# Optimization experiments

Measured on AMD Instinct MI355X. Metric: run time of the kernel, lower is better.

The kernel has to match this reference:

```python
import jax, jax.numpy as jnp
import numpy as np

N, G, E, F, H = 65536, 32768, 600000, 128, 128

def _mlp(x, w1, b1, w2, b2):
    # Linear -> SiLU -> Linear
    return jax.nn.silu(x @ w1 + b1) @ w2 + b2

def setup_inputs() -> dict:
    key = jax.random.key(0)
    ks = jax.random.split(key, 24)
    def lin(k, din, dout):
        kw, kb = jax.random.split(k)
        s = 1.0 / np.sqrt(din)
        return (jax.random.uniform(kw, (din, dout), jnp.float32, -s, s),
                jax.random.uniform(kb, (dout,), jnp.float32, -s, s))
    nm_w1, nm_b1 = lin(ks[0], F, H)
    nm_w2, nm_b2 = lin(ks[1], H, H)
    em_w1, em_b1 = lin(ks[2], 6, H)
    em_w2, em_b2 = lin(ks[3], H, H)
    mm_w1, mm_b1 = lin(ks[4], 2 * H, H)
    mm_w2, mm_b2 = lin(ks[5], H, H)
    um_w1, um_b1 = lin(ks[6], H, H)
    um_w2, um_b2 = lin(ks[7], H, H)
    return {
        "node_features": jax.random.normal(ks[8], (N, F), jnp.float32),
        "node_pos": jax.random.uniform(ks[9], (N, 3), jnp.float32),
        "grid_pos": jax.random.uniform(ks[10], (G, 3), jnp.float32),
        "edge_index": jax.random.randint(ks[11], (2, E), 0, G, jnp.int64),
        "nm_w1": nm_w1, "nm_b1": nm_b1, "nm_w2": nm_w2, "nm_b2": nm_b2,
        "em_w1": em_w1, "em_b1": em_b1, "em_w2": em_w2, "em_b2": em_b2,
        "mm_w1": mm_w1, "mm_b1": mm_b1, "mm_w2": mm_w2, "mm_b2": mm_b2,
        "um_w1": um_w1, "um_b1": um_b1, "um_w2": um_w2, "um_b2": um_b2,
    }

def reference(node_features, node_pos, grid_pos, edge_index,
              nm_w1, nm_b1, nm_w2, nm_b2,
              em_w1, em_b1, em_w2, em_b2,
              mm_w1, mm_b1, mm_w2, mm_b2,
              um_w1, um_b1, um_w2, um_b2):
    src, tgt = edge_index[0], edge_index[1]
    # node_model on all points [N,H]
    nf = _mlp(node_features, nm_w1, nm_b1, nm_w2, nm_b2)
    # edge features from gathered positions [E,6] -> [E,H]
    edge_attr = jnp.concatenate([node_pos[src], grid_pos[tgt]], axis=-1)
    ef = _mlp(edge_attr, em_w1, em_b1, em_w2, em_b2)
    # messages [E,2H] -> [E,H]
    msg = _mlp(jnp.concatenate([nf[src], ef], axis=-1), mm_w1, mm_b1, mm_w2, mm_b2)
    # scatter-add mean aggregation to grid [G,H]
    counts = jax.ops.segment_sum(jnp.ones((msg.shape[0],), msg.dtype), tgt, num_segments=G)
    counts = jnp.maximum(counts, 1.0)[:, None]
    agg = jax.ops.segment_sum(msg, tgt, num_segments=G) / counts
    # update_model [G,H]
    return _mlp(agg, um_w1, um_b1, um_w2, um_b2)
```

## Files before the change

kernel.cpp:

```cpp
#include <hip/hip_runtime.h>

#define N_NODES 65536
#define G_GRID  32768
#define E_EDGES 600000
#define HD      128

typedef __attribute__((ext_vector_type(8))) short bf8;
typedef __attribute__((ext_vector_type(4))) float f32x4;
typedef __attribute__((ext_vector_type(4))) unsigned u32x4;

__device__ __forceinline__ short f2bf(float f){
  union { float f; unsigned u; } v; v.f = f;
  unsigned r = v.u + 0x7FFFu + ((v.u >> 16) & 1u);
  return (short)(r >> 16);
}
__device__ __forceinline__ float bf2f(short s){
  union { unsigned u; float f; } v; v.u = ((unsigned)(unsigned short)s) << 16; return v.f;
}
__device__ __forceinline__ float fsilu(float v){
  return v * __builtin_amdgcn_rcpf(1.f + __expf(-v));
}
__device__ __forceinline__ unsigned cvt_pk_bf16(float lo, float hi){
  unsigned r;
  asm("v_cvt_pk_bf16_f32 %0, %1, %2" : "=v"(r) : "v"(lo), "v"(hi));
  return r;
}

__device__ __forceinline__ bf8 load_pack8(const float* p, float scale){
  float4 u0 = *(const float4*)p;
  float4 u1 = *(const float4*)(p + 4);
  u32x4 pk;
  pk[0] = cvt_pk_bf16(u0.x*scale, u0.y*scale);
  pk[1] = cvt_pk_bf16(u0.z*scale, u0.w*scale);
  pk[2] = cvt_pk_bf16(u1.x*scale, u1.y*scale);
  pk[3] = cvt_pk_bf16(u1.z*scale, u1.w*scale);
  return *(const bf8*)&pk;
}

__global__ void setup_k(const float* __restrict__ nmw1, const float* __restrict__ nmw2,
                        const float* __restrict__ mmw1, const float* __restrict__ mmw2,
                        const float* __restrict__ umw1, const float* __restrict__ umw2,
                        const float* __restrict__ emw1, const float* __restrict__ eb1,
                        const float* __restrict__ emw2, const float* __restrict__ eb2,
                        const float* __restrict__ mb1,
                        const int* __restrict__ eidx,
                        short* __restrict__ wts, short* __restrict__ wcombot,
                        float* __restrict__ bcombo, short* __restrict__ ew1x,
                        int* __restrict__ counts)
{
  const int b = blockIdx.x;
  if (b < 512){
    int i = b*256 + threadIdx.x;
    const float* src; int local; bool k256 = false;
    if      (i < 16384){ src = nmw1; local = i; }
    else if (i < 32768){ src = nmw2; local = i - 16384; }
    else if (i < 49152){ src = emw2; local = i - 32768; }
    else if (i < 81920){ src = mmw1; local = i - 49152; k256 = true; }
    else if (i < 98304){ src = mmw2; local = i - 81920; }
    else if (i < 114688){ src = umw1; local = i - 98304; }
    else               { src = umw2; local = i - 114688; }
    int n, k;
    if (k256){ n = local >> 8; k = local & 255; }
    else     { n = local >> 7; k = local & 127; }
    wts[i] = f2bf(src[k*HD + n]);
  } else if (b < 640){
    __shared__ float part[2][128];
    int k = b - 512;
    int t = threadIdx.x, n = t & 127, half = t >> 7;
    float acc = 0.f;
    const float* er = emw2 + k*HD + half*64;
    #pragma unroll 8
    for (int j=0;j<64;j++) acc += er[j] * mmw1[(HD + half*64 + j)*HD + n];
    part[half][n] = acc;
    __syncthreads();
    if (half == 0) wcombot[n*HD + k] = f2bf(part[0][n] + part[1][n]);
  } else if (b == 640){
    int t = threadIdx.x;
    if (t < 128){
      int n = t;
      float acc = mb1[n];
      for (int j=0;j<HD;j++) acc += eb2[j] * mmw1[(HD + j)*HD + n];
      bcombo[n] = acc;
      short v[32];
      #pragma unroll
      for (int i=0;i<32;i++) v[i] = 0;
      #pragma unroll
      for (int i=0;i<6;i++){
        float wv = emw1[i*HD + n];
        short wh = f2bf(wv);
        short wl = f2bf(wv - bf2f(wh));
        v[i] = wh; v[6+i] = wh; v[12+i] = wl;
      }
      float bv = eb1[n];
      short bh = f2bf(bv);
      v[18] = bh; v[19] = f2bf(bv - bf2f(bh));
      #pragma unroll
      for (int i=0;i<32;i++) ew1x[n*32 + i] = v[i];
    }
  } else {
    int e = (b - 641)*256 + threadIdx.x;
    if (e < E_EDGES) atomicAdd(&counts[eidx[E_EDGES + e]], 1);
  }
}

__global__ void node_mlp_k(const float* __restrict__ X,
                           const short* __restrict__ w1t, const float* __restrict__ b1,
                           const short* __restrict__ w2t, const float* __restrict__ b2,
                           short* __restrict__ nf)
{
  __shared__ short hid[64][136];
  const int t = threadIdx.x;
  const int wave = t >> 6, lane = t & 63, l15 = lane & 15, q = lane >> 4;
  const int rw = blockIdx.x*64 + wave*16;

  bf8 a[4];
  const float* xr = X + (size_t)(rw + l15)*HD;
  #pragma unroll
  for (int kt=0; kt<4; kt++) a[kt] = load_pack8(xr + kt*32 + q*8, 1.0f);

  #pragma unroll
  for (int ct=0; ct<8; ct++){
    f32x4 acc = {0.f,0.f,0.f,0.f};
    #pragma unroll
    for (int kt=0; kt<4; kt++){
      bf8 b = *(const bf8*)(w1t + (ct*16 + l15)*HD + kt*32 + q*8);
      acc = __builtin_amdgcn_mfma_f32_16x16x32_bf16(a[kt], b, acc, 0, 0, 0);
    }
    float bias = b1[ct*16 + l15];
    int col = ct*16 + l15;
    unsigned pa = cvt_pk_bf16(fsilu(acc[0]+bias), fsilu(acc[1]+bias));
    unsigned pb = cvt_pk_bf16(fsilu(acc[2]+bias), fsilu(acc[3]+bias));
    hid[wave*16 + q*4 + 0][col] = (short)(pa & 0xFFFFu);
    hid[wave*16 + q*4 + 1][col] = (short)(pa >> 16);
    hid[wave*16 + q*4 + 2][col] = (short)(pb & 0xFFFFu);
    hid[wave*16 + q*4 + 3][col] = (short)(pb >> 16);
  }
  bf8 a2[4];
  #pragma unroll
  for (int kt=0;kt<4;kt++) a2[kt] = *(const bf8*)&hid[wave*16 + l15][kt*32 + q*8];
  #pragma unroll
  for (int ct=0; ct<8; ct++){
    f32x4 acc = {0.f,0.f,0.f,0.f};
    #pragma unroll
    for (int kt=0;kt<4;kt++){
      bf8 b = *(const bf8*)(w2t + (ct*16 + l15)*HD + kt*32 + q*8);
      acc = __builtin_amdgcn_mfma_f32_16x16x32_bf16(a2[kt], b, acc, 0, 0, 0);
    }
    float bias = b2[ct*16 + l15];
    int col = ct*16 + l15;
    unsigned pa = cvt_pk_bf16(acc[0]+bias, acc[1]+bias);
    unsigned pb = cvt_pk_bf16(acc[2]+bias, acc[3]+bias);
    nf[(size_t)(rw + q*4 + 0)*HD + col] = (short)(pa & 0xFFFFu);
    nf[(size_t)(rw + q*4 + 1)*HD + col] = (short)(pa >> 16);
    nf[(size_t)(rw + q*4 + 2)*HD + col] = (short)(pb & 0xFFFFu);
    nf[(size_t)(rw + q*4 + 3)*HD + col] = (short)(pb >> 16);
  }
}

__global__ void scan_k(const int* __restrict__ counts, int* __restrict__ offs){
  __shared__ int part[1024];
  const int t = threadIdx.x;
  const int base = t*32;
  int loc[32];
  int s = 0;
  #pragma unroll
  for (int i=0;i<32;i++){ loc[i] = s; s += counts[base+i]; }
  part[t] = s;
  __syncthreads();
  for (int off=1; off<1024; off<<=1){
    int v = (t>=off) ? part[t-off] : 0;
    __syncthreads();
    part[t] += v;
    __syncthreads();
  }
  int pre = (t==0) ? 0 : part[t-1];
  #pragma unroll
  for (int i=0;i<32;i++) offs[base+i] = pre + loc[i];
  if (t==1023) offs[G_GRID] = pre + s;
}

__global__ void scatter_k(const int* __restrict__ eidx, const int* __restrict__ offs,
                          int* __restrict__ counts,
                          int* __restrict__ srcs_s, int* __restrict__ tgts_s,
                          const float* __restrict__ npos, const float* __restrict__ gpos,
                          float* __restrict__ pos6){
  int e = blockIdx.x*256 + threadIdx.x;
  if (e < E_EDGES){
    int s = eidx[e];
    int g = eidx[E_EDGES + e];
    int slot = offs[g] + atomicSub(&counts[g], 1) - 1;
    srcs_s[slot] = s;
    tgts_s[slot] = g;
    float* pd = pos6 + (size_t)slot*8;
    pd[0]=npos[s*3+0]; pd[1]=npos[s*3+1]; pd[2]=npos[s*3+2];
    pd[3]=gpos[g*3+0]; pd[4]=gpos[g*3+1]; pd[5]=gpos[g*3+2];
    pd[6]=0.f; pd[7]=0.f;
  }
}

__device__ __forceinline__ bf8 build_af(const float p[6], int q){
  short ph[6], pl[6];
  #pragma unroll
  for (int i=0;i<6;i++){
    ph[i] = f2bf(p[i]);
    pl[i] = f2bf(p[i] - bf2f(ph[i]));
  }
  bf8 af = {0,0,0,0,0,0,0,0};
  if (q == 0){
    af[0]=ph[0]; af[1]=ph[1]; af[2]=ph[2]; af[3]=ph[3];
    af[4]=ph[4]; af[5]=ph[5]; af[6]=pl[0]; af[7]=pl[1];
  } else if (q == 1){
    af[0]=pl[2]; af[1]=pl[3]; af[2]=pl[4]; af[3]=pl[5];
    af[4]=ph[0]; af[5]=ph[1]; af[6]=ph[2]; af[7]=ph[3];
  } else if (q == 2){
    af[0]=ph[4]; af[1]=ph[5]; af[2]=(short)0x3F80; af[3]=(short)0x3F80;
  }
  return af;
}

__device__ __forceinline__ void seg_flush32(const f32x4& a0, const f32x4& a1,
                                            unsigned m, int tr0, int tr1,
                                            int q, int col, bool owner,
                                            float* __restrict__ agg)
{
  if (m == 0u){
    float s = ((a0[0]+a0[1]) + (a0[2]+a0[3])) + ((a1[0]+a1[1]) + (a1[2]+a1[3]));
    s += __shfl_xor(s, 16);
    s += __shfl_xor(s, 32);
    int tg = __shfl(tr0, 0);
    if (owner) atomicAdd(&agg[(size_t)tg*HD + col], s);
  } else {
    unsigned mm = m;
    int lo = 0;
    while (true){
      int hi = mm ? (int)__builtin_ctz(mm) : 32;
      float s = 0.f;
      #pragma unroll
      for (int r=0;r<4;r++){
        int row0 = q*4 + r;
        int row1 = 16 + row0;
        s += (row0 >= lo && row0 < hi) ? a0[r] : 0.f;
        s += (row1 >= lo && row1 < hi) ? a1[r] : 0.f;
      }
      s += __shfl_xor(s, 16);
      s += __shfl_xor(s, 32);
      int tg = (lo < 16) ? __shfl(tr0, lo) : __shfl(tr1, lo - 16);
      if (owner) atomicAdd(&agg[(size_t)tg*HD + col], s);
      if (!mm) break;
      lo = hi; mm &= mm - 1;
    }
  }
}

__global__ void __launch_bounds__(256, 3)
edge_msg13_k(const int* __restrict__ srcs_s, const int* __restrict__ tgts_s,
             const float* __restrict__ pos6,
             const short* __restrict__ ew1x, const float* __restrict__ bcombo,
             const short* __restrict__ mw1t, const short* __restrict__ wcombot,
             const short* __restrict__ mw2t,
             const short* __restrict__ nf, float* __restrict__ agg)
{
  __shared__ int tgtl[128];
  __shared__ short hm[128][136];

  const int t = threadIdx.x;
  const int e0 = blockIdx.x*128;
  const int w = t >> 6, lane = t & 63, l15 = lane & 15, q = lane >> 4;
  const int base = e0 + w*32;
  if (base >= E_EDGES) return;

  const int i0 = base + l15;
  const int i1 = base + 16 + l15;
  const int s0 = srcs_s[i0], s1 = srcs_s[i1];

  bf8 an0[4], an1[4];
  {
    const short* n0p = nf + (size_t)s0*HD + q*8;
    const short* n1p = nf + (size_t)s1*HD + q*8;
    #pragma unroll
    for (int kt=0;kt<4;kt++){ an0[kt] = *(const bf8*)(n0p + kt*32); an1[kt] = *(const bf8*)(n1p + kt*32); }
  }
  float pA[6], pB[6];
  {
    const float* pp = pos6 + (size_t)i0*8;
    f32x4 u0 = *(const f32x4*)pp;
    f32x4 u1 = *(const f32x4*)(pp + 4);
    pA[0]=u0[0]; pA[1]=u0[1]; pA[2]=u0[2]; pA[3]=u0[3]; pA[4]=u1[0]; pA[5]=u1[1];
    const float* pq = pos6 + (size_t)i1*8;
    f32x4 v0 = *(const f32x4*)pq;
    f32x4 v1 = *(const f32x4*)(pq + 4);
    pB[0]=v0[0]; pB[1]=v0[1]; pB[2]=v0[2]; pB[3]=v0[3]; pB[4]=v1[0]; pB[5]=v1[1];
  }

  if (lane < 32){
    tgtl[w*32 + lane] = tgts_s[base + lane];
  }

  bf8 af0 = build_af(pA, q);
  bf8 af1 = build_af(pB, q);
  #pragma unroll
  for (int ct=0; ct<8; ct++){
    bf8 bw = *(const bf8*)(ew1x + (ct*16 + l15)*32 + q*8);
    f32x4 h0 = {0.f,0.f,0.f,0.f}, h1 = {0.f,0.f,0.f,0.f};
    h0 = __builtin_amdgcn_mfma_f32_16x16x32_bf16(af0, bw, h0, 0,0,0);
    h1 = __builtin_amdgcn_mfma_f32_16x16x32_bf16(af1, bw, h1, 0,0,0);
    int col = ct*16 + l15;
    unsigned pa = cvt_pk_bf16(fsilu(h0[0]), fsilu(h0[1]));
    unsigned pb = cvt_pk_bf16(fsilu(h0[2]), fsilu(h0[3]));
    hm[w*32 + q*4 + 0][col] = (short)(pa & 0xFFFFu);
    hm[w*32 + q*4 + 1][col] = (short)(pa >> 16);
    hm[w*32 + q*4 + 2][col] = (short)(pb & 0xFFFFu);
    hm[w*32 + q*4 + 3][col] = (short)(pb >> 16);
    unsigned pc = cvt_pk_bf16(fsilu(h1[0]), fsilu(h1[1]));
    unsigned pd = cvt_pk_bf16(fsilu(h1[2]), fsilu(h1[3]));
    hm[w*32 + 16 + q*4 + 0][col] = (short)(pc & 0xFFFFu);
    hm[w*32 + 16 + q*4 + 1][col] = (short)(pc >> 16);
    hm[w*32 + 16 + q*4 + 2][col] = (short)(pd & 0xFFFFu);
    hm[w*32 + 16 + q*4 + 3][col] = (short)(pd >> 16);
  }

  bf8 ah0[4], ah1[4];
  #pragma unroll
  for (int kt=0;kt<4;kt++){
    ah0[kt] = *(const bf8*)&hm[w*32 + l15][kt*32 + q*8];
    ah1[kt] = *(const bf8*)&hm[w*32 + 16 + l15][kt*32 + q*8];
  }
  #pragma unroll
  for (int ct=0; ct<8; ct++){
    bf8 bw1[4], bwc[4];
    #pragma unroll
    for (int kt=0;kt<4;kt++){
      bw1[kt] = *(const bf8*)(mw1t + (ct*16 + l15)*256 + kt*32 + q*8);
      bwc[kt] = *(const bf8*)(wcombot + (ct*16 + l15)*HD + kt*32 + q*8);
    }
    f32x4 acc0 = {0.f,0.f,0.f,0.f}, acc1 = {0.f,0.f,0.f,0.f};
    #pragma unroll
    for (int kt=0;kt<4;kt++){
      acc0 = __builtin_amdgcn_mfma_f32_16x16x32_bf16(an0[kt], bw1[kt], acc0, 0,0,0);
      acc1 = __builtin_amdgcn_mfma_f32_16x16x32_bf16(an1[kt], bw1[kt], acc1, 0,0,0);
    }
    #pragma unroll
    for (int kt=0;kt<4;kt++){
      acc0 = __builtin_amdgcn_mfma_f32_16x16x32_bf16(ah0[kt], bwc[kt], acc0, 0,0,0);
      acc1 = __builtin_amdgcn_mfma_f32_16x16x32_bf16(ah1[kt], bwc[kt], acc1, 0,0,0);
    }
    float bias = bcombo[ct*16 + l15];
    int col = ct*16 + l15;
    unsigned pa = cvt_pk_bf16(fsilu(acc0[0]+bias), fsilu(acc0[1]+bias));
    unsigned pb = cvt_pk_bf16(fsilu(acc0[2]+bias), fsilu(acc0[3]+bias));
    hm[w*32 + q*4 + 0][col] = (short)(pa & 0xFFFFu);
    hm[w*32 + q*4 + 1][col] = (short)(pa >> 16);
    hm[w*32 + q*4 + 2][col] = (short)(pb & 0xFFFFu);
    hm[w*32 + q*4 + 3][col] = (short)(pb >> 16);
    unsigned pc = cvt_pk_bf16(fsilu(acc1[0]+bias), fsilu(acc1[1]+bias));
    unsigned pd = cvt_pk_bf16(fsilu(acc1[2]+bias), fsilu(acc1[3]+bias));
    hm[w*32 + 16 + q*4 + 0][col] = (short)(pc & 0xFFFFu);
    hm[w*32 + 16 + q*4 + 1][col] = (short)(pc >> 16);
    hm[w*32 + 16 + q*4 + 2][col] = (short)(pd & 0xFFFFu);
    hm[w*32 + 16 + q*4 + 3][col] = (short)(pd >> 16);
  }

  bf8 am0[4], am1[4];
  #pragma unroll
  for (int kt=0;kt<4;kt++){
    am0[kt] = *(const bf8*)&hm[w*32 + l15][kt*32 + q*8];
    am1[kt] = *(const bf8*)&hm[w*32 + 16 + l15][kt*32 + q*8];
  }

  const int tr0 = tgtl[w*32 + l15];
  const int tr1 = tgtl[w*32 + 16 + l15];
  unsigned m32;
  {
    int p0 = __shfl_up(tr0, 1);
    int p1 = __shfl_up(tr1, 1);
    unsigned m0 = (unsigned)__ballot(l15 > 0 && tr0 != p0) & 0xFFFFu;
    unsigned m1 = (unsigned)__ballot(l15 > 0 && tr1 != p1) & 0xFFFFu;
    int t15 = __shfl(tr0, 15);
    int t16 = __shfl(tr1, 0);
    m32 = m0 | (m1 << 16) | ((t16 != t15) ? 0x10000u : 0u);
  }

  #pragma unroll
  for (int ct=0; ct<8; ct++){
    bf8 bw[4];
    #pragma unroll
    for (int kt=0;kt<4;kt++)
      bw[kt] = *(const bf8*)(mw2t + (ct*16 + l15)*HD + kt*32 + q*8);
    f32x4 acc0 = {0.f,0.f,0.f,0.f}, acc1 = {0.f,0.f,0.f,0.f};
    #pragma unroll
    for (int kt=0;kt<4;kt++){
      acc0 = __builtin_amdgcn_mfma_f32_16x16x32_bf16(am0[kt], bw[kt], acc0, 0,0,0);
      acc1 = __builtin_amdgcn_mfma_f32_16x16x32_bf16(am1[kt], bw[kt], acc1, 0,0,0);
    }
    const int col = ct*16 + l15;
    const bool owner = (q == (ct & 3));
    seg_flush32(acc0, acc1, m32, tr0, tr1, q, col, owner, agg);
  }
}

__global__ void update_mlp2_k(const float* __restrict__ agg, const int* __restrict__ offs,
                              const short* __restrict__ w1t, const float* __restrict__ b1,
                              const short* __restrict__ w2t, const float* __restrict__ b2,
                              const float* __restrict__ mb2,
                              float* __restrict__ out)
{
  __shared__ short hid[64][136];
  const int t = threadIdx.x;
  const int wave = t >> 6, lane = t & 63, l15 = lane & 15, q = lane >> 4;
  const int rw = blockIdx.x*64 + wave*16;

  int row = rw + l15;
  int cnt = offs[row+1] - offs[row];
  float rcp = __builtin_amdgcn_rcpf(fmaxf((float)cnt, 1.0f));
  float bsc = (cnt > 0) ? 1.0f : 0.0f;
  bf8 a[4];
  const float* ar = agg + (size_t)row*HD;
  #pragma unroll
  for (int kt=0; kt<4; kt++){
    const float* p  = ar  + kt*32 + q*8;
    const float* mp = mb2 + kt*32 + q*8;
    float4 u0 = *(const float4*)p;   float4 u1 = *(const float4*)(p + 4);
    float4 m0v = *(const float4*)mp; float4 m1v = *(const float4*)(mp + 4);
    u32x4 pk;
    pk[0] = cvt_pk_bf16(u0.x*rcp + m0v.x*bsc, u0.y*rcp + m0v.y*bsc);
    pk[1] = cvt_pk_bf16(u0.z*rcp + m0v.z*bsc, u0.w*rcp + m0v.w*bsc);
    pk[2] = cvt_pk_bf16(u1.x*rcp + m1v.x*bsc, u1.y*rcp + m1v.y*bsc);
    pk[3] = cvt_pk_bf16(u1.z*rcp + m1v.z*bsc, u1.w*rcp + m1v.w*bsc);
    a[kt] = *(const bf8*)&pk;
  }

  #pragma unroll
  for (int ct=0; ct<8; ct++){
    f32x4 acc = {0.f,0.f,0.f,0.f};
    #pragma unroll
    for (int kt=0; kt<4; kt++){
      bf8 b = *(const bf8*)(w1t + (ct*16 + l15)*HD + kt*32 + q*8);
      acc = __builtin_amdgcn_mfma_f32_16x16x32_bf16(a[kt], b, acc, 0, 0, 0);
    }
    float bias = b1[ct*16 + l15];
    int col = ct*16 + l15;
    unsigned pa = cvt_pk_bf16(fsilu(acc[0]+bias), fsilu(acc[1]+bias));
    unsigned pb = cvt_pk_bf16(fsilu(acc[2]+bias), fsilu(acc[3]+bias));
    hid[wave*16 + q*4 + 0][col] = (short)(pa & 0xFFFFu);
    hid[wave*16 + q*4 + 1][col] = (short)(pa >> 16);
    hid[wave*16 + q*4 + 2][col] = (short)(pb & 0xFFFFu);
    hid[wave*16 + q*4 + 3][col] = (short)(pb >> 16);
  }
  bf8 a2[4];
  #pragma unroll
  for (int kt=0;kt<4;kt++) a2[kt] = *(const bf8*)&hid[wave*16 + l15][kt*32 + q*8];
  #pragma unroll
  for (int ct=0; ct<8; ct++){
    f32x4 acc = {0.f,0.f,0.f,0.f};
    #pragma unroll
    for (int kt=0;kt<4;kt++){
      bf8 b = *(const bf8*)(w2t + (ct*16 + l15)*HD + kt*32 + q*8);
      acc = __builtin_amdgcn_mfma_f32_16x16x32_bf16(a2[kt], b, acc, 0, 0, 0);
    }
    float bias = b2[ct*16 + l15];
    #pragma unroll
    for (int r=0;r<4;r++)
      out[(size_t)(rw + q*4 + r)*HD + ct*16 + l15] = acc[r] + bias;
  }
}

extern "C" void kernel_launch(void* const* d_in, const int* in_sizes, int n_in,
                              void* d_out, int out_size, void* d_ws, size_t ws_size,
                              hipStream_t stream)
{
  const float* node_features = (const float*)d_in[0];
  const float* node_pos      = (const float*)d_in[1];
  const float* grid_pos      = (const float*)d_in[2];
  const int*   edge_index    = (const int*)d_in[3];
  const float* nm_w1 = (const float*)d_in[4];
  const float* nm_b1 = (const float*)d_in[5];
  const float* nm_w2 = (const float*)d_in[6];
  const float* nm_b2 = (const float*)d_in[7];
  const float* em_w1 = (const float*)d_in[8];
  const float* em_b1 = (const float*)d_in[9];
  const float* em_w2 = (const float*)d_in[10];
  const float* em_b2 = (const float*)d_in[11];
  const float* mm_w1 = (const float*)d_in[12];
  const float* mm_b1 = (const float*)d_in[13];
  const float* mm_w2 = (const float*)d_in[14];
  const float* mm_b2 = (const float*)d_in[15];
  const float* um_w1 = (const float*)d_in[16];
  const float* um_b1 = (const float*)d_in[17];
  const float* um_w2 = (const float*)d_in[18];
  const float* um_b2 = (const float*)d_in[19];
  float* out = (float*)d_out;

  char* ws = (char*)d_ws;
  short* nf     = (short*)ws;
  int*   counts = (int*)  (ws + 16777216ull);
  int*   offs   = (int*)  (ws + 16908288ull);
  short* wts    = (short*)(ws + 17039424ull);
  short* wcombot= (short*)(ws + 17301568ull);
  float* bcombo = (float*)(ws + 17334336ull);
  short* ew1x   = (short*)(ws + 17334848ull);
  int*   srcs_s = (int*)  (ws + 17343040ull);
  int*   tgts_s = (int*)  (ws + 19743040ull);
  float* pos6   = (float*)(ws + 22143040ull);

  short* nmw1t = wts;
  short* nmw2t = wts + 16384;
  short* mmw1t = wts + 49152;
  short* mmw2t = wts + 81920;
  short* umw1t = wts + 98304;
  short* umw2t = wts + 114688;

  float* agg = out;

  (void)hipMemsetAsync(counts, 0, 131072, stream);
  (void)hipMemsetAsync(out, 0, (size_t)G_GRID*HD*4, stream);

  const int count_blocks = (E_EDGES + 255)/256;
  setup_k<<<641 + count_blocks, 256, 0, stream>>>(nm_w1, nm_w2, mm_w1, mm_w2, um_w1, um_w2,
      em_w1, em_b1, em_w2, em_b2, mm_b1, edge_index, wts, wcombot, bcombo, ew1x, counts);
  node_mlp_k<<<G_GRID/64, 256, 0, stream>>>(node_features, nmw1t, nm_b1, nmw2t, nm_b2, nf);
  scan_k<<<1, 1024, 0, stream>>>(counts, offs);
  scatter_k<<<count_blocks, 256, 0, stream>>>(edge_index, offs, counts, srcs_s, tgts_s,
      node_pos, grid_pos, pos6);
  edge_msg13_k<<<(E_EDGES + 127)/128, 256, 0, stream>>>(srcs_s, tgts_s, pos6,
      ew1x, bcombo, mmw1t, wcombot, mmw2t, nf, agg);
  update_mlp2_k<<<G_GRID/64, 256, 0, stream>>>(agg, offs, umw1t, um_b1, umw2t, um_b2, mm_b2, out);
}
```

Before: 466.5 us.

## Fold output zeroing into setup kernel and split node/update MLP columns across waves

Removes the separate memset of the output buffer by adding extra blocks to the setup kernel that write zeros with float4 stores (2985 + 4096 blocks covers G*H floats). The node and update MLP kernels now process 32 rows per block, with pairs of waves splitting the 8 output column tiles, so there are twice as many blocks. A __syncthreads is added because the hidden tile in LDS is now shared between waves. The aim is to cut one launch and raise parallelism and occupancy in the small MLP kernels, at the cost of a block barrier and redundant A-operand loads by both waves of a pair.

```diff
diff --git a/kernel.cpp b/kernel.cpp
--- a/kernel.cpp
+++ b/kernel.cpp
@@ -46,7 +46,7 @@
                         const int* __restrict__ eidx,
                         short* __restrict__ wts, short* __restrict__ wcombot,
                         float* __restrict__ bcombo, short* __restrict__ ew1x,
-                        int* __restrict__ counts)
+                        int* __restrict__ counts, float4* __restrict__ outz)
 {
   const int b = blockIdx.x;
   if (b < 512){
@@ -97,9 +97,13 @@
       #pragma unroll
       for (int i=0;i<32;i++) ew1x[n*32 + i] = v[i];
     }
-  } else {
+  } else if (b < 2985){
     int e = (b - 641)*256 + threadIdx.x;
     if (e < E_EDGES) atomicAdd(&counts[eidx[E_EDGES + e]], 1);
+  } else {
+    int i = (b - 2985)*256 + threadIdx.x;
+    float4 z; z.x = 0.f; z.y = 0.f; z.z = 0.f; z.w = 0.f;
+    outz[i] = z;
   }
 }
 
@@ -108,10 +112,12 @@
                            const short* __restrict__ w2t, const float* __restrict__ b2,
                            short* __restrict__ nf)
 {
-  __shared__ short hid[64][136];
+  __shared__ short hid[32][136];
   const int t = threadIdx.x;
   const int wave = t >> 6, lane = t & 63, l15 = lane & 15, q = lane >> 4;
-  const int rw = blockIdx.x*64 + wave*16;
+  const int rt = wave >> 1;
+  const int h  = wave & 1;
+  const int rw = blockIdx.x*32 + rt*16;
 
   bf8 a[4];
   const float* xr = X + (size_t)(rw + l15)*HD;
@@ -119,7 +125,8 @@
   for (int kt=0; kt<4; kt++) a[kt] = load_pack8(xr + kt*32 + q*8, 1.0f);
 
   #pragma unroll
-  for (int ct=0; ct<8; ct++){
+  for (int c=0; c<4; c++){
+    const int ct = h*4 + c;
     f32x4 acc = {0.f,0.f,0.f,0.f};
     #pragma unroll
     for (int kt=0; kt<4; kt++){
@@ -130,16 +137,18 @@
     int col = ct*16 + l15;
     unsigned pa = cvt_pk_bf16(fsilu(acc[0]+bias), fsilu(acc[1]+bias));
     unsigned pb = cvt_pk_bf16(fsilu(acc[2]+bias), fsilu(acc[3]+bias));
-    hid[wave*16 + q*4 + 0][col] = (short)(pa & 0xFFFFu);
-    hid[wave*16 + q*4 + 1][col] = (short)(pa >> 16);
-    hid[wave*16 + q*4 + 2][col] = (short)(pb & 0xFFFFu);
-    hid[wave*16 + q*4 + 3][col] = (short)(pb >> 16);
-  }
+    hid[rt*16 + q*4 + 0][col] = (short)(pa & 0xFFFFu);
+    hid[rt*16 + q*4 + 1][col] = (short)(pa >> 16);
+    hid[rt*16 + q*4 + 2][col] = (short)(pb & 0xFFFFu);
+    hid[rt*16 + q*4 + 3][col] = (short)(pb >> 16);
+  }
+  __syncthreads();
   bf8 a2[4];
   #pragma unroll
-  for (int kt=0;kt<4;kt++) a2[kt] = *(const bf8*)&hid[wave*16 + l15][kt*32 + q*8];
-  #pragma unroll
-  for (int ct=0; ct<8; ct++){
+  for (int kt=0;kt<4;kt++) a2[kt] = *(const bf8*)&hid[rt*16 + l15][kt*32 + q*8];
+  #pragma unroll
+  for (int c=0; c<4; c++){
+    const int ct = h*4 + c;
     f32x4 acc = {0.f,0.f,0.f,0.f};
     #pragma unroll
     for (int kt=0;kt<4;kt++){
@@ -404,10 +413,12 @@
                               const float* __restrict__ mb2,
                               float* __restrict__ out)
 {
-  __shared__ short hid[64][136];
+  __shared__ short hid[32][136];
   const int t = threadIdx.x;
   const int wave = t >> 6, lane = t & 63, l15 = lane & 15, q = lane >> 4;
-  const int rw = blockIdx.x*64 + wave*16;
+  const int rt = wave >> 1;
+  const int h  = wave & 1;
+  const int rw = blockIdx.x*32 + rt*16;
 
   int row = rw + l15;
   int cnt = offs[row+1] - offs[row];
@@ -430,7 +441,8 @@
   }
 
   #pragma unroll
-  for (int ct=0; ct<8; ct++){
+  for (int c=0; c<4; c++){
+    const int ct = h*4 + c;
     f32x4 acc = {0.f,0.f,0.f,0.f};
     #pragma unroll
     for (int kt=0; kt<4; kt++){
@@ -441,16 +453,18 @@
     int col = ct*16 + l15;
     unsigned pa = cvt_pk_bf16(fsilu(acc[0]+bias), fsilu(acc[1]+bias));
     unsigned pb = cvt_pk_bf16(fsilu(acc[2]+bias), fsilu(acc[3]+bias));
-    hid[wave*16 + q*4 + 0][col] = (short)(pa & 0xFFFFu);
-    hid[wave*16 + q*4 + 1][col] = (short)(pa >> 16);
-    hid[wave*16 + q*4 + 2][col] = (short)(pb & 0xFFFFu);
-    hid[wave*16 + q*4 + 3][col] = (short)(pb >> 16);
-  }
+    hid[rt*16 + q*4 + 0][col] = (short)(pa & 0xFFFFu);
+    hid[rt*16 + q*4 + 1][col] = (short)(pa >> 16);
+    hid[rt*16 + q*4 + 2][col] = (short)(pb & 0xFFFFu);
+    hid[rt*16 + q*4 + 3][col] = (short)(pb >> 16);
+  }
+  __syncthreads();
   bf8 a2[4];
   #pragma unroll
-  for (int kt=0;kt<4;kt++) a2[kt] = *(const bf8*)&hid[wave*16 + l15][kt*32 + q*8];
-  #pragma unroll
-  for (int ct=0; ct<8; ct++){
+  for (int kt=0;kt<4;kt++) a2[kt] = *(const bf8*)&hid[rt*16 + l15][kt*32 + q*8];
+  #pragma unroll
+  for (int c=0; c<4; c++){
+    const int ct = h*4 + c;
     f32x4 acc = {0.f,0.f,0.f,0.f};
     #pragma unroll
     for (int kt=0;kt<4;kt++){
@@ -512,16 +526,15 @@
   float* agg = out;
 
   (void)hipMemsetAsync(counts, 0, 131072, stream);
-  (void)hipMemsetAsync(out, 0, (size_t)G_GRID*HD*4, stream);
-
-  const int count_blocks = (E_EDGES + 255)/256;
-  setup_k<<<641 + count_blocks, 256, 0, stream>>>(nm_w1, nm_w2, mm_w1, mm_w2, um_w1, um_w2,
-      em_w1, em_b1, em_w2, em_b2, mm_b1, edge_index, wts, wcombot, bcombo, ew1x, counts);
-  node_mlp_k<<<G_GRID/64, 256, 0, stream>>>(node_features, nmw1t, nm_b1, nmw2t, nm_b2, nf);
+
+  setup_k<<<7081, 256, 0, stream>>>(nm_w1, nm_w2, mm_w1, mm_w2, um_w1, um_w2,
+      em_w1, em_b1, em_w2, em_b2, mm_b1, edge_index, wts, wcombot, bcombo, ew1x,
+      counts, (float4*)out);
+  node_mlp_k<<<G_GRID/32, 256, 0, stream>>>(node_features, nmw1t, nm_b1, nmw2t, nm_b2, nf);
   scan_k<<<1, 1024, 0, stream>>>(counts, offs);
-  scatter_k<<<count_blocks, 256, 0, stream>>>(edge_index, offs, counts, srcs_s, tgts_s,
+  scatter_k<<<(E_EDGES + 255)/256, 256, 0, stream>>>(edge_index, offs, counts, srcs_s, tgts_s,
       node_pos, grid_pos, pos6);
   edge_msg13_k<<<(E_EDGES + 127)/128, 256, 0, stream>>>(srcs_s, tgts_s, pos6,
       ew1x, bcombo, mmw1t, wcombot, mmw2t, nf, agg);
-  update_mlp2_k<<<G_GRID/64, 256, 0, stream>>>(agg, offs, umw1t, um_b1, umw2t, um_b2, mm_b2, out);
-}
+  update_mlp2_k<<<G_GRID/32, 256, 0, stream>>>(agg, offs, umw1t, um_b1, umw2t, um_b2, mm_b2, out);
+}
```

After: 466.3 us. Within noise of the previous version (-0.0%).
